# Kernel optimization log

Measured on AMD Instinct MI355X. Metric: run time of the kernel, lower is better.

## Reference

```python
import jax, jax.numpy as jnp
import numpy as np

N_CELL = 66
N_SUB = 29934
N = N_CELL + N_SUB  # 30000 nodes
F = 256
E_HALF = 480000
K = 3
LAYERS = 2
BN_EPS = 1e-5


def setup_inputs() -> dict:
    key = jax.random.key(0)
    ks = jax.random.split(key, 8)
    cell_feat = jax.random.normal(ks[0], (N_CELL, F), dtype=jnp.float32)
    sub_feat = jax.random.normal(ks[1], (N_SUB, F), dtype=jnp.float32)
    # interaction_edge builds a symmetric directed edge list: (a,b) and (b,a)
    src = jax.random.randint(ks[2], (E_HALF,), 0, N)
    dst = jax.random.randint(ks[3], (E_HALF,), 0, N)
    edge_index = jnp.stack([jnp.concatenate([src, dst]),
                            jnp.concatenate([dst, src])], axis=0)
    ew_half = jax.random.uniform(ks[4], (E_HALF,), dtype=jnp.float32, minval=0.1, maxval=1.0)
    edge_weight = jnp.concatenate([ew_half, ew_half])
    glorot = np.sqrt(6.0 / (F + F))
    W1 = jax.random.uniform(ks[5], (F, F), dtype=jnp.float32, minval=-glorot, maxval=glorot)
    W2 = jax.random.uniform(ks[6], (F, F), dtype=jnp.float32, minval=-glorot, maxval=glorot)
    b1 = jnp.zeros((F,), jnp.float32)
    b2 = jnp.zeros((F,), jnp.float32)
    prelu_w = jnp.full((F,), 0.25, jnp.float32)  # PReLU default init
    gamma = jnp.ones((F,), jnp.float32)
    beta = jnp.zeros((F,), jnp.float32)
    return {"cell_feat": cell_feat, "sub_feat": sub_feat,
            "edge_index": edge_index, "edge_weight": edge_weight,
            "W1": W1, "b1": b1, "W2": W2, "b2": b2,
            "prelu_w": prelu_w, "gamma": gamma, "beta": beta}


def _gcn_norm(edge_index, edge_weight, n):
    # SGConv's gcn_norm: add self-loops (weight 1), symmetric degree normalization
    loop = jnp.arange(n)
    row = jnp.concatenate([edge_index[0], loop])  # source j
    col = jnp.concatenate([edge_index[1], loop])  # target i
    ew = jnp.concatenate([edge_weight, jnp.ones((n,), edge_weight.dtype)])
    deg = jax.ops.segment_sum(ew, col, num_segments=n)
    dinv = jnp.where(deg > 0, jax.lax.rsqrt(deg), 0.0)
    norm = dinv[row] * ew * dinv[col]
    return row, col, norm


def _sgconv(x, row, col, norm, W, b, n):
    # K-hop propagation: x <- A_hat^K x, then linear
    for _ in range(K):
        x = jax.ops.segment_sum(norm[:, None] * x[row], col, num_segments=n)
    return x @ W.T + b


def _prelu_bn(x, prelu_w, gamma, beta):
    x = jnp.where(x >= 0, x, prelu_w * x)
    mean = jnp.mean(x, axis=0)
    var = jnp.mean(jnp.square(x - mean), axis=0)  # biased, training-mode BN
    return gamma * (x - mean) * jax.lax.rsqrt(var + BN_EPS) + beta


def reference(cell_feat, sub_feat, edge_index, edge_weight,
              W1, b1, W2, b2, prelu_w, gamma, beta):
    x = jnp.concatenate([cell_feat, sub_feat], axis=0)  # [N, F]
    n = x.shape[0]
    row, col, norm = _gcn_norm(edge_index, edge_weight, n)
    for W, b in ((W1, b1), (W2, b2)):
        x = _sgconv(x, row, col, norm, W, b, n)
        x = _prelu_bn(x, prelu_w, gamma, beta)
    return x[:N_CELL, :], x[N_CELL:, :]
```

## Files before the change

### kernel.cpp

```cpp
#include <hip/hip_runtime.h>
#include <hip/hip_bf16.h>

constexpr int NN    = 30000;
constexpr int NCELL = 66;
constexpr int NF    = 256;
constexpr float EPS = 1e-5f;

using bf16x8 = __attribute__((ext_vector_type(8))) short;
using f32x4  = __attribute__((ext_vector_type(4))) float;

__device__ __forceinline__ float bf2f(unsigned short u) {
    return __uint_as_float(((unsigned)u) << 16);
}
__device__ __forceinline__ unsigned short f2bf(float f) {
    __hip_bfloat16 h = __float2bfloat16(f);
    return *reinterpret_cast<unsigned short*>(&h);
}
__device__ __forceinline__ void acc8(float* acc, float4 u, float w) {
    unsigned a = __float_as_uint(u.x), b = __float_as_uint(u.y);
    unsigned c = __float_as_uint(u.z), d = __float_as_uint(u.w);
    acc[0] += w * __uint_as_float(a << 16);
    acc[1] += w * __uint_as_float(a & 0xffff0000u);
    acc[2] += w * __uint_as_float(b << 16);
    acc[3] += w * __uint_as_float(b & 0xffff0000u);
    acc[4] += w * __uint_as_float(c << 16);
    acc[5] += w * __uint_as_float(c & 0xffff0000u);
    acc[6] += w * __uint_as_float(d << 16);
    acc[7] += w * __uint_as_float(d & 0xffff0000u);
}

__global__ void k_init(unsigned long long* packed, int* fill, float* sums) {
    int i = blockIdx.x * 256 + threadIdx.x;
    if (i < NN) { packed[i] = 0ull; fill[i] = 0; }
    if (i < 2 * NF) sums[i] = 0.0f;
}

__global__ void k_zero_stats(float* sums) {
    int i = threadIdx.x;
    if (i < 2 * NF) sums[i] = 0.0f;
}

__global__ void k_concat_h(const float4* __restrict__ cell, const float4* __restrict__ sub,
                           ushort4* __restrict__ xh) {
    int idx = blockIdx.x * 256 + threadIdx.x;
    if (idx >= NN * (NF / 4)) return;
    const int CELL4 = NCELL * (NF / 4);
    float4 v = (idx < CELL4) ? cell[idx] : sub[idx - CELL4];
    ushort4 o;
    o.x = f2bf(v.x); o.y = f2bf(v.y); o.z = f2bf(v.z); o.w = f2bf(v.w);
    xh[idx] = o;
}

__global__ void k_cvtw(const float4* __restrict__ W, ushort4* __restrict__ Wh) {
    int idx = blockIdx.x * 256 + threadIdx.x;
    if (idx >= NF * NF / 4) return;
    float4 v = W[idx];
    ushort4 o;
    o.x = f2bf(v.x); o.y = f2bf(v.y); o.z = f2bf(v.z); o.w = f2bf(v.w);
    Wh[idx] = o;
}

__global__ void k_pass1(const int* __restrict__ ei, const float* __restrict__ ew,
                        unsigned long long* packed, int E) {
    int e = blockIdx.x * 256 + threadIdx.x;
    if (e >= E) return;
    int col = ei[E + e];
    unsigned long long p = (1ull << 40) |
        (unsigned long long)__float2uint_rn(ew[e] * 16777216.0f);
    atomicAdd(&packed[col], p);
}

__global__ void k_dinv(const unsigned long long* __restrict__ packed,
                       float* __restrict__ dinv, int* __restrict__ counts) {
    int i = blockIdx.x * 256 + threadIdx.x;
    if (i >= NN) return;
    unsigned long long p = packed[i];
    counts[i] = (int)(p >> 40);
    float deg = 1.0f + (float)((double)(p & 0xFFFFFFFFFFull) * 5.9604644775390625e-8);
    dinv[i] = rsqrtf(deg);
}

__global__ void k_scan(const int* __restrict__ counts, int* __restrict__ col_ptr) {
    __shared__ int part[256];
    __shared__ int pref[257];
    int t = threadIdx.x;
    const int CH = (NN + 255) / 256;
    int beg = t * CH;
    int end = beg + CH; if (end > NN) end = NN;
    int s = 0;
    for (int i = beg; i < end; i++) s += counts[i];
    part[t] = s;
    __syncthreads();
    if (t == 0) {
        int r = 0;
        for (int i = 0; i < 256; i++) { pref[i] = r; r += part[i]; }
        pref[256] = r;
    }
    __syncthreads();
    int run = pref[t];
    for (int i = beg; i < end; i++) { col_ptr[i] = run; run += counts[i]; }
    if (t == 255) col_ptr[NN] = pref[256];
}

__global__ void k_scatter(const int* __restrict__ ei, const float* __restrict__ ew,
                          const float* __restrict__ dinv, const int* __restrict__ col_ptr,
                          int* fill, int* __restrict__ rs, float* __restrict__ ns, int E) {
    int e = blockIdx.x * 256 + threadIdx.x;
    if (e >= E) return;
    int row = ei[e];
    int col = ei[E + e];
    float nrm = dinv[row] * ew[e] * dinv[col];
    int pos = col_ptr[col] + atomicAdd(&fill[col], 1);
    rs[pos] = row;
    ns[pos] = nrm;
}

__global__ __launch_bounds__(256) void k_prop(const ushort* __restrict__ xin,
                                              ushort* __restrict__ xout,
                                              const int* __restrict__ col_ptr,
                                              const int* __restrict__ rs,
                                              const float* __restrict__ ns,
                                              const float* __restrict__ dinv) {
    int n = blockIdx.x * 4 + (threadIdx.x >> 6);
    int lane = threadIdx.x & 63;
    int half = lane >> 5;
    int fb = lane & 31;
    const float4* xrow = (const float4*)xin;
    int beg = col_ptr[n], end = col_ptr[n + 1];
    int cnt = end - beg;
    float acc[8];
    #pragma unroll
    for (int i = 0; i < 8; i++) acc[i] = 0.f;
    int steps = cnt >> 1;
    int it = 0;
    int e = beg + half;
    for (; it + 8 <= steps; it += 8, e += 16) {
        int   s0 = rs[e],      s1 = rs[e + 2],  s2 = rs[e + 4],  s3 = rs[e + 6];
        int   s4 = rs[e + 8],  s5 = rs[e + 10], s6 = rs[e + 12], s7 = rs[e + 14];
        float w0 = ns[e],      w1 = ns[e + 2],  w2 = ns[e + 4],  w3 = ns[e + 6];
        float w4 = ns[e + 8],  w5 = ns[e + 10], w6 = ns[e + 12], w7 = ns[e + 14];
        float4 u0 = xrow[s0 * 32 + fb];
        float4 u1 = xrow[s1 * 32 + fb];
        float4 u2 = xrow[s2 * 32 + fb];
        float4 u3 = xrow[s3 * 32 + fb];
        float4 u4 = xrow[s4 * 32 + fb];
        float4 u5 = xrow[s5 * 32 + fb];
        float4 u6 = xrow[s6 * 32 + fb];
        float4 u7 = xrow[s7 * 32 + fb];
        acc8(acc, u0, w0); acc8(acc, u1, w1); acc8(acc, u2, w2); acc8(acc, u3, w3);
        acc8(acc, u4, w4); acc8(acc, u5, w5); acc8(acc, u6, w6); acc8(acc, u7, w7);
    }
    for (; it + 4 <= steps; it += 4, e += 8) {
        int   s0 = rs[e],     s1 = rs[e + 2], s2 = rs[e + 4], s3 = rs[e + 6];
        float w0 = ns[e],     w1 = ns[e + 2], w2 = ns[e + 4], w3 = ns[e + 6];
        float4 u0 = xrow[s0 * 32 + fb];
        float4 u1 = xrow[s1 * 32 + fb];
        float4 u2 = xrow[s2 * 32 + fb];
        float4 u3 = xrow[s3 * 32 + fb];
        acc8(acc, u0, w0); acc8(acc, u1, w1); acc8(acc, u2, w2); acc8(acc, u3, w3);
    }
    for (; it < steps; ++it, e += 2) {
        int s0 = rs[e]; float w0 = ns[e];
        float4 u0 = xrow[s0 * 32 + fb];
        acc8(acc, u0, w0);
    }
    if ((cnt & 1) && half == 0) {
        int el = beg + cnt - 1;
        float4 u0 = xrow[rs[el] * 32 + fb];
        acc8(acc, u0, ns[el]);
    }
    #pragma unroll
    for (int i = 0; i < 8; i++) acc[i] += __shfl_xor(acc[i], 32);
    if (half == 0) {
        float dn = dinv[n];
        float4 u = xrow[n * 32 + fb];
        acc8(acc, u, dn * dn);
        unsigned p0 = ((unsigned)f2bf(acc[1]) << 16) | f2bf(acc[0]);
        unsigned p1 = ((unsigned)f2bf(acc[3]) << 16) | f2bf(acc[2]);
        unsigned p2 = ((unsigned)f2bf(acc[5]) << 16) | f2bf(acc[4]);
        unsigned p3 = ((unsigned)f2bf(acc[7]) << 16) | f2bf(acc[6]);
        float4 o;
        o.x = __uint_as_float(p0); o.y = __uint_as_float(p1);
        o.z = __uint_as_float(p2); o.w = __uint_as_float(p3);
        ((float4*)xout)[n * 32 + fb] = o;
    }
}

__global__ __launch_bounds__(256) void k_gemm_fused(const short* __restrict__ A,
                                                    const short* __restrict__ B,
                                                    const float* __restrict__ bias,
                                                    const float* __restrict__ pw,
                                                    float* __restrict__ y,
                                                    float* __restrict__ sums) {
    constexpr int RT = NN / 16;
    int w    = threadIdx.x >> 6;
    int lane = threadIdx.x & 63;
    int rt   = blockIdx.x * 4 + w;
    int ml   = lane & 15;
    int q    = lane >> 4;
    bool valid = rt < RT;
    __shared__ float red[2][4][NF];
    f32x4 acc[16];
    #pragma unroll
    for (int i = 0; i < 16; i++) acc[i] = (f32x4){0.f, 0.f, 0.f, 0.f};
    if (valid) {
        const short* arow = A + (rt * 16 + ml) * NF + q * 8;
        #pragma unroll
        for (int ks = 0; ks < 8; ks++) {
            bf16x8 a = *(const bf16x8*)(arow + ks * 32);
            #pragma unroll
            for (int nt = 0; nt < 16; nt++) {
                bf16x8 b = *(const bf16x8*)(B + (nt * 16 + ml) * NF + ks * 32 + q * 8);
                acc[nt] = __builtin_amdgcn_mfma_f32_16x16x32_bf16(a, b, acc[nt], 0, 0, 0);
            }
        }
    }
    #pragma unroll
    for (int nt = 0; nt < 16; nt++) {
        int col = nt * 16 + ml;
        float s = 0.f, s2 = 0.f;
        if (valid) {
            float bb = bias[col];
            float pc = pw[col];
            #pragma unroll
            for (int r = 0; r < 4; r++) {
                float v = acc[nt][r] + bb;
                v = (v >= 0.f) ? v : pc * v;
                s += v; s2 += v * v;
                y[(rt * 16 + q * 4 + r) * NF + col] = v;
            }
        }
        s  += __shfl_xor(s, 16);  s  += __shfl_xor(s, 32);
        s2 += __shfl_xor(s2, 16); s2 += __shfl_xor(s2, 32);
        if (lane < 16) { red[0][w][col] = s; red[1][w][col] = s2; }
    }
    __syncthreads();
    int t = threadIdx.x;
    float v0 = red[0][0][t] + red[0][1][t] + red[0][2][t] + red[0][3][t];
    float v1 = red[1][0][t] + red[1][1][t] + red[1][2][t] + red[1][3][t];
    atomicAdd(&sums[t], v0);
    atomicAdd(&sums[NF + t], v1);
}

__global__ void k_finalize(const float* __restrict__ sums, const float* __restrict__ gamma,
                           const float* __restrict__ beta, float* __restrict__ ss) {
    int t = threadIdx.x;
    float mean = sums[t] / (float)NN;
    float var = sums[NF + t] / (float)NN - mean * mean;
    if (var < 0.f) var = 0.f;
    float istd = rsqrtf(var + EPS);
    float sc = gamma[t] * istd;
    ss[t] = sc;
    ss[NF + t] = beta[t] - mean * sc;
}

__global__ void k_apply_h(const float4* __restrict__ y, const float* __restrict__ ss,
                          ushort4* __restrict__ xh) {
    int idx = blockIdx.x * 256 + threadIdx.x;
    if (idx >= NN * (NF / 4)) return;
    int f = (idx & 63) * 4;
    float4 v = y[idx];
    ushort4 o;
    o.x = f2bf(v.x * ss[f]     + ss[NF + f]);
    o.y = f2bf(v.y * ss[f + 1] + ss[NF + f + 1]);
    o.z = f2bf(v.z * ss[f + 2] + ss[NF + f + 2]);
    o.w = f2bf(v.w * ss[f + 3] + ss[NF + f + 3]);
    xh[idx] = o;
}

__global__ void k_apply_out(const float4* __restrict__ y, const float* __restrict__ ss,
                            float4* __restrict__ out) {
    int idx = blockIdx.x * 256 + threadIdx.x;
    if (idx >= NN * (NF / 4)) return;
    int f = (idx & 63) * 4;
    float4 v = y[idx];
    float4 o;
    o.x = v.x * ss[f]     + ss[NF + f];
    o.y = v.y * ss[f + 1] + ss[NF + f + 1];
    o.z = v.z * ss[f + 2] + ss[NF + f + 2];
    o.w = v.w * ss[f + 3] + ss[NF + f + 3];
    out[idx] = o;
}

extern "C" void kernel_launch(void* const* d_in, const int* in_sizes, int n_in,
                              void* d_out, int out_size, void* d_ws, size_t ws_size,
                              hipStream_t stream) {
    const float* cell  = (const float*)d_in[0];
    const float* sub   = (const float*)d_in[1];
    const int*   ei    = (const int*)  d_in[2];
    const float* ew    = (const float*)d_in[3];
    const float* W1    = (const float*)d_in[4];
    const float* bias1 = (const float*)d_in[5];
    const float* W2    = (const float*)d_in[6];
    const float* bias2 = (const float*)d_in[7];
    const float* pw    = (const float*)d_in[8];
    const float* gamma = (const float*)d_in[9];
    const float* beta  = (const float*)d_in[10];
    float* out = (float*)d_out;
    const int E = in_sizes[3];

    char* ws = (char*)d_ws;
    size_t off = 0;
    auto alloc = [&](size_t bytes) -> void* {
        void* p = ws + off;
        off = (off + bytes + 255) & ~((size_t)255);
        return p;
    };
    ushort* xh0    = (ushort*)alloc((size_t)NN * NF * 2);
    ushort* xh1    = (ushort*)alloc((size_t)NN * NF * 2);
    float*  yf     = (float*) alloc((size_t)NN * NF * 4);
    ushort* W1h    = (ushort*)alloc((size_t)NF * NF * 2);
    ushort* W2h    = (ushort*)alloc((size_t)NF * NF * 2);
    unsigned long long* packed = (unsigned long long*)alloc((size_t)NN * 8);
    float*  dinv   = (float*) alloc((size_t)NN * 4);
    int*    counts = (int*)   alloc((size_t)NN * 4);
    int*    col_ptr= (int*)   alloc((size_t)(NN + 1) * 4);
    int*    fill   = (int*)   alloc((size_t)NN * 4);
    int*    rs     = (int*)   alloc((size_t)E * 4);
    float*  ns     = (float*) alloc((size_t)E * 4);
    float*  sums   = (float*) alloc((size_t)2 * NF * 4);
    float*  ss     = (float*) alloc((size_t)2 * NF * 4);

    const int gN  = (NN + 255) / 256;
    const int gE  = (E + 255) / 256;
    const int gV4 = (NN * NF / 4 + 255) / 256;
    const int gW4 = (NF * NF / 4 + 255) / 256;
    const int gP  = NN / 4;
    const int gG  = (NN / 16 + 3) / 4;

    k_init<<<gN, 256, 0, stream>>>(packed, fill, sums);
    k_concat_h<<<gV4, 256, 0, stream>>>((const float4*)cell, (const float4*)sub, (ushort4*)xh0);
    k_cvtw<<<gW4, 256, 0, stream>>>((const float4*)W1, (ushort4*)W1h);
    k_cvtw<<<gW4, 256, 0, stream>>>((const float4*)W2, (ushort4*)W2h);
    k_pass1<<<gE, 256, 0, stream>>>(ei, ew, packed, E);
    k_dinv<<<gN, 256, 0, stream>>>(packed, dinv, counts);
    k_scan<<<1, 256, 0, stream>>>(counts, col_ptr);
    k_scatter<<<gE, 256, 0, stream>>>(ei, ew, dinv, col_ptr, fill, rs, ns, E);

    k_prop<<<gP, 256, 0, stream>>>(xh0, xh1, col_ptr, rs, ns, dinv);
    k_prop<<<gP, 256, 0, stream>>>(xh1, xh0, col_ptr, rs, ns, dinv);
    k_prop<<<gP, 256, 0, stream>>>(xh0, xh1, col_ptr, rs, ns, dinv);
    k_gemm_fused<<<gG, 256, 0, stream>>>((const short*)xh1, (const short*)W1h, bias1, pw, yf, sums);
    k_finalize<<<1, 256, 0, stream>>>(sums, gamma, beta, ss);
    k_apply_h<<<gV4, 256, 0, stream>>>((const float4*)yf, ss, (ushort4*)xh0);
    k_zero_stats<<<1, 512, 0, stream>>>(sums);

    k_prop<<<gP, 256, 0, stream>>>(xh0, xh1, col_ptr, rs, ns, dinv);
    k_prop<<<gP, 256, 0, stream>>>(xh1, xh0, col_ptr, rs, ns, dinv);
    k_prop<<<gP, 256, 0, stream>>>(xh0, xh1, col_ptr, rs, ns, dinv);
    k_gemm_fused<<<gG, 256, 0, stream>>>((const short*)xh1, (const short*)W2h, bias2, pw, yf, sums);
    k_finalize<<<1, 256, 0, stream>>>(sums, gamma, beta, ss);
    k_apply_out<<<gV4, 256, 0, stream>>>((const float4*)yf, ss, (float4*)out);
}
```

Measured before the change: 723.1 us.

## Split propagation into feature chunks and pack edge index/weight pairs

Each SpMM hop now runs as four launches, each handling a 64-feature slice. A wave processes 8 edges in parallel with 8 lanes per edge instead of 2 edges with 32 lanes, which is meant to shrink the gathered working set per pass so it stays in cache. Row index and normalized weight are packed into one 64-bit word, loaded and stored nontemporally. In exchange, the edge metadata is re-read four times per hop, there are more kernel launches, and the reduction needs three shuffle stages.

```diff
diff --git a/kernel.cpp b/kernel.cpp
--- a/kernel.cpp
+++ b/kernel.cpp
@@ -27,6 +27,11 @@
     acc[5] += w * __uint_as_float(c & 0xffff0000u);
     acc[6] += w * __uint_as_float(d << 16);
     acc[7] += w * __uint_as_float(d & 0xffff0000u);
+}
+__device__ __forceinline__ void edge_meta(const long long* p, int& r, float& w) {
+    long long v = __builtin_nontemporal_load(p);
+    r = (int)(unsigned)(v & 0xffffffffll);
+    w = __int_as_float((int)(v >> 32));
 }
 
 __global__ void k_init(unsigned long long* packed, int* fill, float* sums) {
@@ -104,76 +109,61 @@
 
 __global__ void k_scatter(const int* __restrict__ ei, const float* __restrict__ ew,
                           const float* __restrict__ dinv, const int* __restrict__ col_ptr,
-                          int* fill, int* __restrict__ rs, float* __restrict__ ns, int E) {
+                          int* fill, long long* __restrict__ rsns, int E) {
     int e = blockIdx.x * 256 + threadIdx.x;
     if (e >= E) return;
     int row = ei[e];
     int col = ei[E + e];
     float nrm = dinv[row] * ew[e] * dinv[col];
     int pos = col_ptr[col] + atomicAdd(&fill[col], 1);
-    rs[pos] = row;
-    ns[pos] = nrm;
+    long long pv = ((long long)__float_as_int(nrm) << 32) | (unsigned)row;
+    __builtin_nontemporal_store(pv, &rsns[pos]);
 }
 
 __global__ __launch_bounds__(256) void k_prop(const ushort* __restrict__ xin,
                                               ushort* __restrict__ xout,
                                               const int* __restrict__ col_ptr,
-                                              const int* __restrict__ rs,
-                                              const float* __restrict__ ns,
-                                              const float* __restrict__ dinv) {
+                                              const long long* __restrict__ rsns,
+                                              const float* __restrict__ dinv,
+                                              int chunk) {
     int n = blockIdx.x * 4 + (threadIdx.x >> 6);
     int lane = threadIdx.x & 63;
-    int half = lane >> 5;
-    int fb = lane & 31;
+    int g  = lane >> 3;
+    int fl = lane & 7;
+    int fo = chunk * 8 + fl;
     const float4* xrow = (const float4*)xin;
     int beg = col_ptr[n], end = col_ptr[n + 1];
-    int cnt = end - beg;
     float acc[8];
     #pragma unroll
     for (int i = 0; i < 8; i++) acc[i] = 0.f;
-    int steps = cnt >> 1;
-    int it = 0;
-    int e = beg + half;
-    for (; it + 8 <= steps; it += 8, e += 16) {
-        int   s0 = rs[e],      s1 = rs[e + 2],  s2 = rs[e + 4],  s3 = rs[e + 6];
-        int   s4 = rs[e + 8],  s5 = rs[e + 10], s6 = rs[e + 12], s7 = rs[e + 14];
-        float w0 = ns[e],      w1 = ns[e + 2],  w2 = ns[e + 4],  w3 = ns[e + 6];
-        float w4 = ns[e + 8],  w5 = ns[e + 10], w6 = ns[e + 12], w7 = ns[e + 14];
-        float4 u0 = xrow[s0 * 32 + fb];
-        float4 u1 = xrow[s1 * 32 + fb];
-        float4 u2 = xrow[s2 * 32 + fb];
-        float4 u3 = xrow[s3 * 32 + fb];
-        float4 u4 = xrow[s4 * 32 + fb];
-        float4 u5 = xrow[s5 * 32 + fb];
-        float4 u6 = xrow[s6 * 32 + fb];
-        float4 u7 = xrow[s7 * 32 + fb];
+    int e = beg + g;
+    for (; e + 24 < end; e += 32) {
+        int r0, r1, r2, r3; float w0, w1, w2, w3;
+        edge_meta(&rsns[e],      r0, w0);
+        edge_meta(&rsns[e + 8],  r1, w1);
+        edge_meta(&rsns[e + 16], r2, w2);
+        edge_meta(&rsns[e + 24], r3, w3);
+        float4 u0 = xrow[r0 * 32 + fo];
+        float4 u1 = xrow[r1 * 32 + fo];
+        float4 u2 = xrow[r2 * 32 + fo];
+        float4 u3 = xrow[r3 * 32 + fo];
         acc8(acc, u0, w0); acc8(acc, u1, w1); acc8(acc, u2, w2); acc8(acc, u3, w3);
-        acc8(acc, u4, w4); acc8(acc, u5, w5); acc8(acc, u6, w6); acc8(acc, u7, w7);
-    }
-    for (; it + 4 <= steps; it += 4, e += 8) {
-        int   s0 = rs[e],     s1 = rs[e + 2], s2 = rs[e + 4], s3 = rs[e + 6];
-        float w0 = ns[e],     w1 = ns[e + 2], w2 = ns[e + 4], w3 = ns[e + 6];
-        float4 u0 = xrow[s0 * 32 + fb];
-        float4 u1 = xrow[s1 * 32 + fb];
-        float4 u2 = xrow[s2 * 32 + fb];
-        float4 u3 = xrow[s3 * 32 + fb];
-        acc8(acc, u0, w0); acc8(acc, u1, w1); acc8(acc, u2, w2); acc8(acc, u3, w3);
-    }
-    for (; it < steps; ++it, e += 2) {
-        int s0 = rs[e]; float w0 = ns[e];
-        float4 u0 = xrow[s0 * 32 + fb];
+    }
+    for (; e < end; e += 8) {
+        int r0; float w0;
+        edge_meta(&rsns[e], r0, w0);
+        float4 u0 = xrow[r0 * 32 + fo];
         acc8(acc, u0, w0);
     }
-    if ((cnt & 1) && half == 0) {
-        int el = beg + cnt - 1;
-        float4 u0 = xrow[rs[el] * 32 + fb];
-        acc8(acc, u0, ns[el]);
-    }
     #pragma unroll
-    for (int i = 0; i < 8; i++) acc[i] += __shfl_xor(acc[i], 32);
-    if (half == 0) {
+    for (int i = 0; i < 8; i++) {
+        acc[i] += __shfl_xor(acc[i], 8);
+        acc[i] += __shfl_xor(acc[i], 16);
+        acc[i] += __shfl_xor(acc[i], 32);
+    }
+    if (g == 0) {
         float dn = dinv[n];
-        float4 u = xrow[n * 32 + fb];
+        float4 u = xrow[n * 32 + fo];
         acc8(acc, u, dn * dn);
         unsigned p0 = ((unsigned)f2bf(acc[1]) << 16) | f2bf(acc[0]);
         unsigned p1 = ((unsigned)f2bf(acc[3]) << 16) | f2bf(acc[2]);
@@ -182,7 +172,7 @@
         float4 o;
         o.x = __uint_as_float(p0); o.y = __uint_as_float(p1);
         o.z = __uint_as_float(p2); o.w = __uint_as_float(p3);
-        ((float4*)xout)[n * 32 + fb] = o;
+        ((float4*)xout)[n * 32 + fo] = o;
     }
 }
 
@@ -316,8 +306,7 @@
     int*    counts = (int*)   alloc((size_t)NN * 4);
     int*    col_ptr= (int*)   alloc((size_t)(NN + 1) * 4);
     int*    fill   = (int*)   alloc((size_t)NN * 4);
-    int*    rs     = (int*)   alloc((size_t)E * 4);
-    float*  ns     = (float*) alloc((size_t)E * 4);
+    long long* rsns= (long long*)alloc((size_t)E * 8);
     float*  sums   = (float*) alloc((size_t)2 * NF * 4);
     float*  ss     = (float*) alloc((size_t)2 * NF * 4);
 
@@ -327,6 +316,11 @@
     const int gW4 = (NF * NF / 4 + 255) / 256;
     const int gP  = NN / 4;
     const int gG  = (NN / 16 + 3) / 4;
+
+    auto hop = [&](ushort* xin, ushort* xout) {
+        for (int c = 0; c < 4; c++)
+            k_prop<<<gP, 256, 0, stream>>>(xin, xout, col_ptr, rsns, dinv, c);
+    };
 
     k_init<<<gN, 256, 0, stream>>>(packed, fill, sums);
     k_concat_h<<<gV4, 256, 0, stream>>>((const float4*)cell, (const float4*)sub, (ushort4*)xh0);
@@ -335,19 +329,19 @@
     k_pass1<<<gE, 256, 0, stream>>>(ei, ew, packed, E);
     k_dinv<<<gN, 256, 0, stream>>>(packed, dinv, counts);
     k_scan<<<1, 256, 0, stream>>>(counts, col_ptr);
-    k_scatter<<<gE, 256, 0, stream>>>(ei, ew, dinv, col_ptr, fill, rs, ns, E);
-
-    k_prop<<<gP, 256, 0, stream>>>(xh0, xh1, col_ptr, rs, ns, dinv);
-    k_prop<<<gP, 256, 0, stream>>>(xh1, xh0, col_ptr, rs, ns, dinv);
-    k_prop<<<gP, 256, 0, stream>>>(xh0, xh1, col_ptr, rs, ns, dinv);
+    k_scatter<<<gE, 256, 0, stream>>>(ei, ew, dinv, col_ptr, fill, rsns, E);
+
+    hop(xh0, xh1);
+    hop(xh1, xh0);
+    hop(xh0, xh1);
     k_gemm_fused<<<gG, 256, 0, stream>>>((const short*)xh1, (const short*)W1h, bias1, pw, yf, sums);
     k_finalize<<<1, 256, 0, stream>>>(sums, gamma, beta, ss);
     k_apply_h<<<gV4, 256, 0, stream>>>((const float4*)yf, ss, (ushort4*)xh0);
     k_zero_stats<<<1, 512, 0, stream>>>(sums);
 
-    k_prop<<<gP, 256, 0, stream>>>(xh0, xh1, col_ptr, rs, ns, dinv);
-    k_prop<<<gP, 256, 0, stream>>>(xh1, xh0, col_ptr, rs, ns, dinv);
-    k_prop<<<gP, 256, 0, stream>>>(xh0, xh1, col_ptr, rs, ns, dinv);
+    hop(xh0, xh1);
+    hop(xh1, xh0);
+    hop(xh0, xh1);
     k_gemm_fused<<<gG, 256, 0, stream>>>((const short*)xh1, (const short*)W2h, bias2, pw, yf, sums);
     k_finalize<<<1, 256, 0, stream>>>(sums, gamma, beta, ss);
     k_apply_out<<<gV4, 256, 0, stream>>>((const float4*)yf, ss, (float4*)out);
```

Result: slower. 980.3 us (+35.6%).

## Replace CSR scan with atomic segment allocation and pack edge metadata

Applied to the files above, without the earlier changes.

Drops the single-block serial prefix scan and gives each node its CSR segment through an atomicAdd on a global cursor, storing separate begin and end arrays. Edge source index and normalized weight are packed into one 64-bit word, so the propagation kernel does one load per edge instead of two. These loads use nontemporal hints. Segment order becomes nondeterministic, which can hurt locality between neighbouring nodes' edge lists, and the 8-byte stride loads across the two half-waves may coalesce less well.

```diff
diff --git a/kernel.cpp b/kernel.cpp
--- a/kernel.cpp
+++ b/kernel.cpp
@@ -28,11 +28,17 @@
     acc[6] += w * __uint_as_float(d << 16);
     acc[7] += w * __uint_as_float(d & 0xffff0000u);
 }
-
-__global__ void k_init(unsigned long long* packed, int* fill, float* sums) {
+__device__ __forceinline__ void edge_meta(const long long* p, int& r, float& w) {
+    long long v = __builtin_nontemporal_load(p);
+    r = (int)(unsigned)(v & 0xffffffffll);
+    w = __int_as_float((int)(v >> 32));
+}
+
+__global__ void k_init(unsigned long long* packed, int* fill, float* sums, int* cursor) {
     int i = blockIdx.x * 256 + threadIdx.x;
     if (i < NN) { packed[i] = 0ull; fill[i] = 0; }
     if (i < 2 * NF) sums[i] = 0.0f;
+    if (i == 0) *cursor = 0;
 }
 
 __global__ void k_zero_stats(float* sums) {
@@ -71,62 +77,45 @@
 }
 
 __global__ void k_dinv(const unsigned long long* __restrict__ packed,
-                       float* __restrict__ dinv, int* __restrict__ counts) {
+                       float* __restrict__ dinv,
+                       int* __restrict__ col_beg, int* __restrict__ col_end,
+                       int* cursor) {
     int i = blockIdx.x * 256 + threadIdx.x;
     if (i >= NN) return;
     unsigned long long p = packed[i];
-    counts[i] = (int)(p >> 40);
+    int cnt = (int)(p >> 40);
     float deg = 1.0f + (float)((double)(p & 0xFFFFFFFFFFull) * 5.9604644775390625e-8);
     dinv[i] = rsqrtf(deg);
-}
-
-__global__ void k_scan(const int* __restrict__ counts, int* __restrict__ col_ptr) {
-    __shared__ int part[256];
-    __shared__ int pref[257];
-    int t = threadIdx.x;
-    const int CH = (NN + 255) / 256;
-    int beg = t * CH;
-    int end = beg + CH; if (end > NN) end = NN;
-    int s = 0;
-    for (int i = beg; i < end; i++) s += counts[i];
-    part[t] = s;
-    __syncthreads();
-    if (t == 0) {
-        int r = 0;
-        for (int i = 0; i < 256; i++) { pref[i] = r; r += part[i]; }
-        pref[256] = r;
-    }
-    __syncthreads();
-    int run = pref[t];
-    for (int i = beg; i < end; i++) { col_ptr[i] = run; run += counts[i]; }
-    if (t == 255) col_ptr[NN] = pref[256];
+    int pos = atomicAdd(cursor, cnt);
+    col_beg[i] = pos;
+    col_end[i] = pos + cnt;
 }
 
 __global__ void k_scatter(const int* __restrict__ ei, const float* __restrict__ ew,
-                          const float* __restrict__ dinv, const int* __restrict__ col_ptr,
-                          int* fill, int* __restrict__ rs, float* __restrict__ ns, int E) {
+                          const float* __restrict__ dinv, const int* __restrict__ col_beg,
+                          int* fill, long long* __restrict__ rsns, int E) {
     int e = blockIdx.x * 256 + threadIdx.x;
     if (e >= E) return;
     int row = ei[e];
     int col = ei[E + e];
     float nrm = dinv[row] * ew[e] * dinv[col];
-    int pos = col_ptr[col] + atomicAdd(&fill[col], 1);
-    rs[pos] = row;
-    ns[pos] = nrm;
+    int pos = col_beg[col] + atomicAdd(&fill[col], 1);
+    long long pv = ((long long)__float_as_int(nrm) << 32) | (unsigned)row;
+    __builtin_nontemporal_store(pv, &rsns[pos]);
 }
 
 __global__ __launch_bounds__(256) void k_prop(const ushort* __restrict__ xin,
                                               ushort* __restrict__ xout,
-                                              const int* __restrict__ col_ptr,
-                                              const int* __restrict__ rs,
-                                              const float* __restrict__ ns,
+                                              const int* __restrict__ col_beg,
+                                              const int* __restrict__ col_end,
+                                              const long long* __restrict__ rsns,
                                               const float* __restrict__ dinv) {
     int n = blockIdx.x * 4 + (threadIdx.x >> 6);
     int lane = threadIdx.x & 63;
     int half = lane >> 5;
     int fb = lane & 31;
     const float4* xrow = (const float4*)xin;
-    int beg = col_ptr[n], end = col_ptr[n + 1];
+    int beg = col_beg[n], end = col_end[n];
     int cnt = end - beg;
     float acc[8];
     #pragma unroll
@@ -135,39 +124,50 @@
     int it = 0;
     int e = beg + half;
     for (; it + 8 <= steps; it += 8, e += 16) {
-        int   s0 = rs[e],      s1 = rs[e + 2],  s2 = rs[e + 4],  s3 = rs[e + 6];
-        int   s4 = rs[e + 8],  s5 = rs[e + 10], s6 = rs[e + 12], s7 = rs[e + 14];
-        float w0 = ns[e],      w1 = ns[e + 2],  w2 = ns[e + 4],  w3 = ns[e + 6];
-        float w4 = ns[e + 8],  w5 = ns[e + 10], w6 = ns[e + 12], w7 = ns[e + 14];
-        float4 u0 = xrow[s0 * 32 + fb];
-        float4 u1 = xrow[s1 * 32 + fb];
-        float4 u2 = xrow[s2 * 32 + fb];
-        float4 u3 = xrow[s3 * 32 + fb];
-        float4 u4 = xrow[s4 * 32 + fb];
-        float4 u5 = xrow[s5 * 32 + fb];
-        float4 u6 = xrow[s6 * 32 + fb];
-        float4 u7 = xrow[s7 * 32 + fb];
+        int r0, r1, r2, r3, r4, r5, r6, r7;
+        float w0, w1, w2, w3, w4, w5, w6, w7;
+        edge_meta(&rsns[e],      r0, w0);
+        edge_meta(&rsns[e + 2],  r1, w1);
+        edge_meta(&rsns[e + 4],  r2, w2);
+        edge_meta(&rsns[e + 6],  r3, w3);
+        edge_meta(&rsns[e + 8],  r4, w4);
+        edge_meta(&rsns[e + 10], r5, w5);
+        edge_meta(&rsns[e + 12], r6, w6);
+        edge_meta(&rsns[e + 14], r7, w7);
+        float4 u0 = xrow[r0 * 32 + fb];
+        float4 u1 = xrow[r1 * 32 + fb];
+        float4 u2 = xrow[r2 * 32 + fb];
+        float4 u3 = xrow[r3 * 32 + fb];
+        float4 u4 = xrow[r4 * 32 + fb];
+        float4 u5 = xrow[r5 * 32 + fb];
+        float4 u6 = xrow[r6 * 32 + fb];
+        float4 u7 = xrow[r7 * 32 + fb];
         acc8(acc, u0, w0); acc8(acc, u1, w1); acc8(acc, u2, w2); acc8(acc, u3, w3);
         acc8(acc, u4, w4); acc8(acc, u5, w5); acc8(acc, u6, w6); acc8(acc, u7, w7);
     }
     for (; it + 4 <= steps; it += 4, e += 8) {
-        int   s0 = rs[e],     s1 = rs[e + 2], s2 = rs[e + 4], s3 = rs[e + 6];
-        float w0 = ns[e],     w1 = ns[e + 2], w2 = ns[e + 4], w3 = ns[e + 6];
-        float4 u0 = xrow[s0 * 32 + fb];
-        float4 u1 = xrow[s1 * 32 + fb];
-        float4 u2 = xrow[s2 * 32 + fb];
-        float4 u3 = xrow[s3 * 32 + fb];
+        int r0, r1, r2, r3; float w0, w1, w2, w3;
+        edge_meta(&rsns[e],     r0, w0);
+        edge_meta(&rsns[e + 2], r1, w1);
+        edge_meta(&rsns[e + 4], r2, w2);
+        edge_meta(&rsns[e + 6], r3, w3);
+        float4 u0 = xrow[r0 * 32 + fb];
+        float4 u1 = xrow[r1 * 32 + fb];
+        float4 u2 = xrow[r2 * 32 + fb];
+        float4 u3 = xrow[r3 * 32 + fb];
         acc8(acc, u0, w0); acc8(acc, u1, w1); acc8(acc, u2, w2); acc8(acc, u3, w3);
     }
     for (; it < steps; ++it, e += 2) {
-        int s0 = rs[e]; float w0 = ns[e];
-        float4 u0 = xrow[s0 * 32 + fb];
+        int r0; float w0;
+        edge_meta(&rsns[e], r0, w0);
+        float4 u0 = xrow[r0 * 32 + fb];
         acc8(acc, u0, w0);
     }
     if ((cnt & 1) && half == 0) {
-        int el = beg + cnt - 1;
-        float4 u0 = xrow[rs[el] * 32 + fb];
-        acc8(acc, u0, ns[el]);
+        int r0; float w0;
+        edge_meta(&rsns[beg + cnt - 1], r0, w0);
+        float4 u0 = xrow[r0 * 32 + fb];
+        acc8(acc, u0, w0);
     }
     #pragma unroll
     for (int i = 0; i < 8; i++) acc[i] += __shfl_xor(acc[i], 32);
@@ -313,13 +313,13 @@
     ushort* W2h    = (ushort*)alloc((size_t)NF * NF * 2);
     unsigned long long* packed = (unsigned long long*)alloc((size_t)NN * 8);
     float*  dinv   = (float*) alloc((size_t)NN * 4);
-    int*    counts = (int*)   alloc((size_t)NN * 4);
-    int*    col_ptr= (int*)   alloc((size_t)(NN + 1) * 4);
+    int*    col_beg= (int*)   alloc((size_t)NN * 4);
+    int*    col_end= (int*)   alloc((size_t)NN * 4);
     int*    fill   = (int*)   alloc((size_t)NN * 4);
-    int*    rs     = (int*)   alloc((size_t)E * 4);
-    float*  ns     = (float*) alloc((size_t)E * 4);
+    long long* rsns= (long long*)alloc((size_t)E * 8);
     float*  sums   = (float*) alloc((size_t)2 * NF * 4);
     float*  ss     = (float*) alloc((size_t)2 * NF * 4);
+    int*    cursor = (int*)   alloc(64);
 
     const int gN  = (NN + 255) / 256;
     const int gE  = (E + 255) / 256;
@@ -328,26 +328,25 @@
     const int gP  = NN / 4;
     const int gG  = (NN / 16 + 3) / 4;
 
-    k_init<<<gN, 256, 0, stream>>>(packed, fill, sums);
+    k_init<<<gN, 256, 0, stream>>>(packed, fill, sums, cursor);
     k_concat_h<<<gV4, 256, 0, stream>>>((const float4*)cell, (const float4*)sub, (ushort4*)xh0);
     k_cvtw<<<gW4, 256, 0, stream>>>((const float4*)W1, (ushort4*)W1h);
     k_cvtw<<<gW4, 256, 0, stream>>>((const float4*)W2, (ushort4*)W2h);
     k_pass1<<<gE, 256, 0, stream>>>(ei, ew, packed, E);
-    k_dinv<<<gN, 256, 0, stream>>>(packed, dinv, counts);
-    k_scan<<<1, 256, 0, stream>>>(counts, col_ptr);
-    k_scatter<<<gE, 256, 0, stream>>>(ei, ew, dinv, col_ptr, fill, rs, ns, E);
-
-    k_prop<<<gP, 256, 0, stream>>>(xh0, xh1, col_ptr, rs, ns, dinv);
-    k_prop<<<gP, 256, 0, stream>>>(xh1, xh0, col_ptr, rs, ns, dinv);
-    k_prop<<<gP, 256, 0, stream>>>(xh0, xh1, col_ptr, rs, ns, dinv);
+    k_dinv<<<gN, 256, 0, stream>>>(packed, dinv, col_beg, col_end, cursor);
+    k_scatter<<<gE, 256, 0, stream>>>(ei, ew, dinv, col_beg, fill, rsns, E);
+
+    k_prop<<<gP, 256, 0, stream>>>(xh0, xh1, col_beg, col_end, rsns, dinv);
+    k_prop<<<gP, 256, 0, stream>>>(xh1, xh0, col_beg, col_end, rsns, dinv);
+    k_prop<<<gP, 256, 0, stream>>>(xh0, xh1, col_beg, col_end, rsns, dinv);
     k_gemm_fused<<<gG, 256, 0, stream>>>((const short*)xh1, (const short*)W1h, bias1, pw, yf, sums);
     k_finalize<<<1, 256, 0, stream>>>(sums, gamma, beta, ss);
     k_apply_h<<<gV4, 256, 0, stream>>>((const float4*)yf, ss, (ushort4*)xh0);
     k_zero_stats<<<1, 512, 0, stream>>>(sums);
 
-    k_prop<<<gP, 256, 0, stream>>>(xh0, xh1, col_ptr, rs, ns, dinv);
-    k_prop<<<gP, 256, 0, stream>>>(xh1, xh0, col_ptr, rs, ns, dinv);
-    k_prop<<<gP, 256, 0, stream>>>(xh0, xh1, col_ptr, rs, ns, dinv);
+    k_prop<<<gP, 256, 0, stream>>>(xh0, xh1, col_beg, col_end, rsns, dinv);
+    k_prop<<<gP, 256, 0, stream>>>(xh1, xh0, col_beg, col_end, rsns, dinv);
+    k_prop<<<gP, 256, 0, stream>>>(xh0, xh1, col_beg, col_end, rsns, dinv);
     k_gemm_fused<<<gG, 256, 0, stream>>>((const short*)xh1, (const short*)W2h, bias2, pw, yf, sums);
     k_finalize<<<1, 256, 0, stream>>>(sums, gamma, beta, ss);
     k_apply_out<<<gV4, 256, 0, stream>>>((const float4*)yf, ss, (float4*)out);
```

Result: no change. 722.5 us (-0.1%).
